# Optimization experiments

Hardware: AMD Instinct MI355X
Metric: run time of the kernel (lower is better)

The kernel has to match this reference:

```python
import jax, jax.numpy as jnp
import numpy as np

IH, IW = 14, 14
NUM_HEADS = 16
HEAD_DIMS = 32
INP_DIMS = 512
B = 128


def make_relative_position_index(ih, iw):
    coords = np.stack(np.meshgrid(np.arange(ih), np.arange(iw), indexing='ij'))  # [2, ih, iw]
    cf = coords.reshape(2, -1)  # [2, n]
    rel = cf[:, :, None] - cf[:, None, :]  # [2, n, n]
    rel = rel.transpose(1, 2, 0)  # [n, n, 2]
    rel[:, :, 0] += ih - 1
    rel[:, :, 1] += iw - 1
    rel[:, :, 0] *= 2 * iw - 1
    return rel.sum(-1).astype(np.int64)  # [n, n]


def setup_inputs() -> dict:
    key = jax.random.key(0)
    k1, k2, k3, k4, k5 = jax.random.split(key, 5)
    n = IH * IW
    inner = NUM_HEADS * HEAD_DIMS
    x = jax.random.normal(k1, (B, n, INP_DIMS), dtype=jnp.float32)
    qkv_w = jax.random.normal(k2, (INP_DIMS, 3 * inner), dtype=jnp.float32) * 0.02
    rel_bias_table = jax.random.normal(k3, ((2 * IH - 1) * (2 * IW - 1), NUM_HEADS), dtype=jnp.float32) * 0.02
    proj_w = jax.random.normal(k4, (inner, INP_DIMS), dtype=jnp.float32) * 0.02
    proj_b = jax.random.normal(k5, (INP_DIMS,), dtype=jnp.float32) * 0.02
    rel_pos_index = jnp.asarray(make_relative_position_index(IH, IW))
    return {"x": x, "qkv_w": qkv_w, "rel_bias_table": rel_bias_table,
            "proj_w": proj_w, "proj_b": proj_b, "rel_pos_index": rel_pos_index}


def reference(x, qkv_w, rel_bias_table, proj_w, proj_b, rel_pos_index):
    b, n, c = x.shape
    h, hd = NUM_HEADS, HEAD_DIMS
    scale = (INP_DIMS // NUM_HEADS) ** (-0.5)
    qkv = x @ qkv_w  # [b, n, 3*h*hd]
    qkv = qkv.reshape(b, n, 3, h, hd).transpose(2, 0, 3, 1, 4)  # [3, b, h, n, hd]
    q, k, v = qkv[0] * scale, qkv[1], qkv[2]
    attn = jnp.einsum('bhqd,bhkd->bhqk', q, k)  # [b, h, n, n]
    # gather relative position bias: [n*n, h] -> [h, n, n]
    bias = rel_bias_table[rel_pos_index.reshape(-1)].reshape(n, n, h).transpose(2, 0, 1)
    attn = jax.nn.softmax(attn + bias[None], axis=-1)
    out = jnp.einsum('bhqk,bhkd->bhqd', attn, v)  # [b, h, n, hd]
    out = out.transpose(0, 2, 1, 3).reshape(b, n, h * hd)
    return out @ proj_w + proj_b
```

## Files before the change

### kernel.cpp

```cpp
#include <hip/hip_runtime.h>

#define NTOK 196
#define QPAD 208
#define KP 208
#define PSTR 232
#define VKP 208

typedef __attribute__((ext_vector_type(8))) short short8;
typedef __attribute__((ext_vector_type(4))) short short4_t;
typedef __attribute__((ext_vector_type(4))) float float4_t;

__device__ __forceinline__ short f2bf(float f) {
  unsigned u = __float_as_uint(f);
  u = (u + 0x7fffu + ((u >> 16) & 1u)) >> 16;
  return (short)u;
}

__global__ __launch_bounds__(256) void fill_kernel(float* __restrict__ out,
                                                   int n) {
  int i = blockIdx.x * 256 + threadIdx.x;
  if (i < n) out[i] = 1000.0f;
}

__global__ __launch_bounds__(256) void cvt_kernel(const float* __restrict__ in,
                                                  short* __restrict__ out) {
  int i = (blockIdx.x * 256 + threadIdx.x) * 8;
  float4_t a = *(const float4_t*)&in[i];
  float4_t b = *(const float4_t*)&in[i + 4];
  short8 v;
  v[0] = f2bf(a[0]); v[1] = f2bf(a[1]); v[2] = f2bf(a[2]); v[3] = f2bf(a[3]);
  v[4] = f2bf(b[0]); v[5] = f2bf(b[1]); v[6] = f2bf(b[2]); v[7] = f2bf(b[3]);
  *(short8*)&out[i] = v;
}

__device__ __forceinline__ void transpose_body(const float* __restrict__ in,
                                               short* __restrict__ out, int R,
                                               int C, int bx, int by,
                                               float (*tile)[65]) {
  int c0 = bx * 64, r0 = by * 64;
  int tc = threadIdx.x & 63, tr = threadIdx.x >> 6;
#pragma unroll
  for (int s = 0; s < 16; s++) {
    int r = s * 4 + tr;
    tile[r][tc] = in[(r0 + r) * C + c0 + tc];
  }
  __syncthreads();
#pragma unroll
  for (int s = 0; s < 16; s++) {
    int i = s * 4 + tr;
    out[(c0 + i) * R + r0 + tc] = f2bf(tile[tc][i]);
  }
}

__global__ __launch_bounds__(256) void prep_kernel(
    const float* __restrict__ qkv_w, const float* __restrict__ proj_w,
    const float* __restrict__ table, const int* __restrict__ rpi,
    short* __restrict__ wt1, short* __restrict__ wt2, float* __restrict__ bias,
    short* __restrict__ vb, int do_vpad) {
  __shared__ float tile[64][65];
  int blk = blockIdx.x;
  if (blk < 192) {
    transpose_body(qkv_w, wt1, 512, 1536, blk % 24, blk / 24, tile);
  } else if (blk < 256) {
    int i = blk - 192;
    transpose_body(proj_w, wt2, 512, 512, i % 8, i / 8, tile);
  } else if (blk < 2960) {
    int idx = (blk - 256) * 256 + threadIdx.x;
    int h = idx / (QPAD * KP);
    int rem = idx % (QPAD * KP);
    int q = rem / KP, k = rem % KP;
    float v = 0.f;
    if (q < NTOK && k < NTOK) v = table[rpi[q * NTOK + k] * 16 + h];
    bias[idx] = v;
  } else if (do_vpad) {
    int i = (blk - 2960) * 256 + threadIdx.x;
    int row = i / 3, g = i - 3 * (i / 3);
    short4_t z = {0, 0, 0, 0};
    *(short4_t*)&vb[row * VKP + 196 + g * 4] = z;
  }
}

__device__ __forceinline__ void gemm_tile(const short* __restrict__ A,
                                          const short* __restrict__ B, int K,
                                          int m0, int n0, short (*As)[72],
                                          short (*Bs)[72], float4_t acc[4][4]) {
  int tid = threadIdx.x;
  int lane = tid & 63, wave = tid >> 6;
  int quad = lane >> 4, l16 = lane & 15;
  int wm = (wave >> 1) * 64, wn = (wave & 1) * 64;
  int srow = tid >> 3, scol = (tid & 7) * 8;
  for (int k0 = 0; k0 < K; k0 += 64) {
#pragma unroll
    for (int i = 0; i < 4; i++) {
      int r = srow + i * 32;
      *(short8*)&As[r][scol] = *(const short8*)&A[(m0 + r) * K + k0 + scol];
      *(short8*)&Bs[r][scol] = *(const short8*)&B[(n0 + r) * K + k0 + scol];
    }
    __syncthreads();
#pragma unroll
    for (int ks = 0; ks < 2; ks++) {
      short8 af[4], bfr[4];
#pragma unroll
      for (int i = 0; i < 4; i++) {
        af[i] = *(short8*)&As[wm + i * 16 + l16][ks * 32 + quad * 8];
        bfr[i] = *(short8*)&Bs[wn + i * 16 + l16][ks * 32 + quad * 8];
      }
#pragma unroll
      for (int mi = 0; mi < 4; mi++)
#pragma unroll
        for (int ni = 0; ni < 4; ni++)
          acc[mi][ni] = __builtin_amdgcn_mfma_f32_16x16x32_bf16(
              af[mi], bfr[ni], acc[mi][ni], 0, 0, 0);
    }
    __syncthreads();
  }
}

__global__ __launch_bounds__(256) void qkv_gemm(
    const short* __restrict__ xb, const short* __restrict__ wt1,
    short* __restrict__ qb, short* __restrict__ kb, short* __restrict__ vb) {
  __shared__ __align__(16) short As[128][72];
  __shared__ __align__(16) short Bs[128][72];
  float4_t acc[4][4];
  float4_t z = {0.f, 0.f, 0.f, 0.f};
#pragma unroll
  for (int i = 0; i < 4; i++)
#pragma unroll
    for (int j = 0; j < 4; j++) acc[i][j] = z;
  int lin = blockIdx.x + blockIdx.y * 12;
  int xcd = lin & 7, loc = lin >> 3;
  int nl = xcd * 294 + loc;
  int bx = nl % 12, by = nl / 12;
  int m0 = by * 128, n0 = bx * 128;
  gemm_tile(xb, wt1, 512, m0, n0, As, Bs, acc);
  int lane = threadIdx.x & 63, wave = threadIdx.x >> 6;
  int quad = lane >> 4, l16 = lane & 15;
  int wm = (wave >> 1) * 64, wn = (wave & 1) * 64;
  const float qscale = 0.17677669529663687f;
#pragma unroll
  for (int mi = 0; mi < 4; mi++)
#pragma unroll
    for (int ni = 0; ni < 4; ni++) {
      int colg = n0 + wn + ni * 16 + l16;
      int s = colg >> 9, rem = colg & 511;
      int h = rem >> 5, d = rem & 31;
      int rowg0 = m0 + wm + mi * 16 + quad * 4;
      if (s == 2) {
        int b = rowg0 / NTOK, nt = rowg0 - b * NTOK;
        short4_t v4;
        v4[0] = f2bf(acc[mi][ni][0]);
        v4[1] = f2bf(acc[mi][ni][1]);
        v4[2] = f2bf(acc[mi][ni][2]);
        v4[3] = f2bf(acc[mi][ni][3]);
        *(short4_t*)&vb[((b * 16 + h) * 32 + d) * VKP + nt] = v4;
      } else {
#pragma unroll
        for (int r = 0; r < 4; r++) {
          int rowg = rowg0 + r;
          int b = rowg / NTOK, n = rowg - b * NTOK;
          int off = ((b * 16 + h) * QPAD + n) * 32 + d;
          if (s == 0)
            qb[off] = f2bf(acc[mi][ni][r] * qscale);
          else
            kb[off] = f2bf(acc[mi][ni][r]);
        }
      }
    }
}

__global__ __launch_bounds__(512) void attn_kernel(
    const short* __restrict__ qb, const short* __restrict__ kb,
    const short* __restrict__ vb, const float* __restrict__ bias,
    short* __restrict__ aout) {
  __shared__ __align__(16) short vT[32][PSTR];
  __shared__ __align__(16) short P[8][16][PSTR];
  int bh = blockIdx.x, b = bh >> 4, h = bh & 15;
  int tid = threadIdx.x, wave = tid >> 6, lane = tid & 63;
  int quad = lane >> 4, l16 = lane & 15;
  int base_row = b * NTOK;
  const short* vsrc = vb + bh * 32 * VKP;
  for (int i = tid; i < 32 * 26; i += 512) {
    int d = i / 26, c = (i - d * 26) * 8;
    *(short8*)&vT[d][c] = *(const short8*)&vsrc[d * VKP + c];
  }
  short8 z8 = {0, 0, 0, 0, 0, 0, 0, 0};
  if (tid < 32 * 3) {
    int d = tid / 3, c = 208 + (tid - d * 3) * 8;
    *(short8*)&vT[d][c] = z8;
  }
  __syncthreads();
  float4_t z4 = {0.f, 0.f, 0.f, 0.f};
  for (int i2 = 0; i2 < 2; i2++) {
    int qt = wave + 8 * i2;
    if (qt > 12) break;
    int qr0 = qt * 16;
    short8 qf = *(const short8*)&qb[(bh * QPAD + qr0 + l16) * 32 + quad * 8];
    float4_t s[13];
#pragma unroll
    for (int kt = 0; kt < 13; kt++) {
      short8 kf =
          *(const short8*)&kb[(bh * QPAD + kt * 16 + l16) * 32 + quad * 8];
      s[kt] = __builtin_amdgcn_mfma_f32_16x16x32_bf16(qf, kf, z4, 0, 0, 0);
    }
    const float* brow = bias + (h * QPAD + qr0 + quad * 4) * KP;
#pragma unroll
    for (int kt = 0; kt < 13; kt++) {
      int col = kt * 16 + l16;
#pragma unroll
      for (int r = 0; r < 4; r++) s[kt][r] += brow[r * KP + col];
    }
    if (l16 >= 4) {
#pragma unroll
      for (int r = 0; r < 4; r++) s[12][r] = -1e30f;
    }
    float invr[4];
#pragma unroll
    for (int r = 0; r < 4; r++) {
      float m = s[0][r];
#pragma unroll
      for (int kt = 1; kt < 13; kt++) m = fmaxf(m, s[kt][r]);
      m = fmaxf(m, __shfl_xor(m, 8, 16));
      m = fmaxf(m, __shfl_xor(m, 4, 16));
      m = fmaxf(m, __shfl_xor(m, 2, 16));
      m = fmaxf(m, __shfl_xor(m, 1, 16));
      float sum = 0.f;
#pragma unroll
      for (int kt = 0; kt < 13; kt++) {
        float p = __expf(s[kt][r] - m);
        s[kt][r] = p;
        sum += p;
      }
      sum += __shfl_xor(sum, 8, 16);
      sum += __shfl_xor(sum, 4, 16);
      sum += __shfl_xor(sum, 2, 16);
      sum += __shfl_xor(sum, 1, 16);
      invr[r] = 1.f / sum;
      short* prow = &P[wave][quad * 4 + r][0];
#pragma unroll
      for (int kt = 0; kt < 13; kt++)
        prow[kt * 16 + l16] = f2bf(s[kt][r]);
      prow[208 + l16] = 0;
    }
    float4_t o0 = z4, o1 = z4;
#pragma unroll
    for (int kt = 0; kt < 7; kt++) {
      short8 pf = *(short8*)&P[wave][l16][kt * 32 + quad * 8];
      short8 vf0 = *(short8*)&vT[l16][kt * 32 + quad * 8];
      short8 vf1 = *(short8*)&vT[16 + l16][kt * 32 + quad * 8];
      o0 = __builtin_amdgcn_mfma_f32_16x16x32_bf16(pf, vf0, o0, 0, 0, 0);
      o1 = __builtin_amdgcn_mfma_f32_16x16x32_bf16(pf, vf1, o1, 0, 0, 0);
    }
#pragma unroll
    for (int r = 0; r < 4; r++) {
      int row = qr0 + quad * 4 + r;
      if (row < NTOK) {
        int off = (base_row + row) * 512 + h * 32;
        aout[off + l16] = f2bf(o0[r] * invr[r]);
        aout[off + 16 + l16] = f2bf(o1[r] * invr[r]);
      }
    }
  }
}

__global__ __launch_bounds__(256, 2) void fused_attn(
    const short* __restrict__ xb, const short* __restrict__ wt1,
    const float* __restrict__ bias, short* __restrict__ aout) {
  __shared__ __align__(16) short R1[64 * PSTR];
  __shared__ __align__(16) short R2[32 * PSTR];
  __shared__ __align__(16) short Qs[224][40];
  __shared__ __align__(16) short Ks[224][40];
  short(*As)[40] = (short(*)[40])R1;
  short(*P)[PSTR] = (short(*)[PSTR])R1;
  short(*Bs)[40] = (short(*)[40])R2;
  short(*vTs)[PSTR] = (short(*)[PSTR])R2;

  int bh = blockIdx.x, b = bh >> 4, h = bh & 15;
  int tid = threadIdx.x, wave = tid >> 6, lane = tid & 63;
  int quad = lane >> 4, l16 = lane & 15;
  int base_row = b * NTOK;

  float4_t z4 = {0.f, 0.f, 0.f, 0.f};
  float4_t acc[4][6];
#pragma unroll
  for (int i = 0; i < 4; i++)
#pragma unroll
    for (int n = 0; n < 6; n++) acc[i][n] = z4;

  int srow = tid >> 2, scol = (tid & 3) * 8;
  for (int k0 = 0; k0 < 512; k0 += 32) {
#pragma unroll
    for (int i = 0; i < 4; i++) {
      int r = srow + i * 64;
      if (r < 224) {
        int gr = base_row + r;
        if (gr > 25087) gr = 25087;
        *(short8*)&As[r][scol] = *(const short8*)&xb[gr * 512 + k0 + scol];
      }
    }
#pragma unroll
    for (int i = 0; i < 2; i++) {
      int r = srow + i * 64;
      if (r < 96) {
        int sec = r >> 5, r32 = r & 31;
        *(short8*)&Bs[r][scol] =
            *(const short8*)&wt1[(sec * 512 + h * 32 + r32) * 512 + k0 + scol];
      }
    }
    __syncthreads();
    short8 af[4], bfv[6];
#pragma unroll
    for (int i = 0; i < 4; i++) {
      int mt = (i < 3) ? (wave + 4 * i) : (12 + (wave & 1));
      af[i] = *(short8*)&As[mt * 16 + l16][quad * 8];
    }
#pragma unroll
    for (int n = 0; n < 6; n++) bfv[n] = *(short8*)&Bs[n * 16 + l16][quad * 8];
#pragma unroll
    for (int i = 0; i < 4; i++)
#pragma unroll
      for (int n = 0; n < 6; n++)
        acc[i][n] = __builtin_amdgcn_mfma_f32_16x16x32_bf16(af[i], bfv[n],
                                                            acc[i][n], 0, 0, 0);
    __syncthreads();
  }
  const float qscale = 0.17677669529663687f;
#pragma unroll
  for (int i = 0; i < 4; i++) {
    if (i == 3 && wave >= 2) break;
    int mt = (i < 3) ? (wave + 4 * i) : (12 + wave);
    int row0 = mt * 16 + quad * 4;
#pragma unroll
    for (int n = 0; n < 6; n++) {
      int c = n * 16 + l16;
#pragma unroll
      for (int r = 0; r < 4; r++) {
        int row = row0 + r;
        float v = acc[i][n][r];
        if (c < 32)
          Qs[row][c] = f2bf(v * qscale);
        else if (c < 64)
          Ks[row][c - 32] = f2bf(v);
        else
          vTs[c - 64][row] = f2bf(v);
      }
    }
  }
  __syncthreads();
  for (int i2 = 0; i2 < 4; i2++) {
    bool active = (i2 < 3) || (wave == 0);
    int qt = (i2 < 3) ? (wave + 4 * i2) : 12;
    int qr0 = qt * 16;
    if (active) {
      short8 qf = *(short8*)&Qs[qr0 + l16][quad * 8];
      float4_t s[13];
#pragma unroll
      for (int kt = 0; kt < 13; kt++) {
        short8 kf = *(short8*)&Ks[kt * 16 + l16][quad * 8];
        s[kt] = __builtin_amdgcn_mfma_f32_16x16x32_bf16(qf, kf, z4, 0, 0, 0);
      }
      const float* brow = bias + (h * QPAD + qr0 + quad * 4) * KP;
#pragma unroll
      for (int kt = 0; kt < 13; kt++) {
        int col = kt * 16 + l16;
#pragma unroll
        for (int r = 0; r < 4; r++) s[kt][r] += brow[r * KP + col];
      }
      if (l16 >= 4) {
#pragma unroll
        for (int r = 0; r < 4; r++) s[12][r] = -1e30f;
      }
      int prow_base = wave * 16 + quad * 4;
#pragma unroll
      for (int r = 0; r < 4; r++) {
        float m = s[0][r];
#pragma unroll
        for (int kt = 1; kt < 13; kt++) m = fmaxf(m, s[kt][r]);
        m = fmaxf(m, __shfl_xor(m, 8, 16));
        m = fmaxf(m, __shfl_xor(m, 4, 16));
        m = fmaxf(m, __shfl_xor(m, 2, 16));
        m = fmaxf(m, __shfl_xor(m, 1, 16));
        float sum = 0.f;
#pragma unroll
        for (int kt = 0; kt < 13; kt++) {
          float p = __expf(s[kt][r] - m);
          s[kt][r] = p;
          sum += p;
        }
        sum += __shfl_xor(sum, 8, 16);
        sum += __shfl_xor(sum, 4, 16);
        sum += __shfl_xor(sum, 2, 16);
        sum += __shfl_xor(sum, 1, 16);
        float inv = 1.f / sum;
        short* prow = &P[prow_base + r][0];
#pragma unroll
        for (int kt = 0; kt < 13; kt++)
          prow[kt * 16 + l16] = f2bf(s[kt][r] * inv);
        prow[208 + l16] = 0;
      }
    }
    __syncthreads();
    if (active) {
      float4_t o0 = z4, o1 = z4;
#pragma unroll
      for (int kt = 0; kt < 7; kt++) {
        short8 pf = *(short8*)&P[wave * 16 + l16][kt * 32 + quad * 8];
        short8 vf0 = *(short8*)&vTs[l16][kt * 32 + quad * 8];
        short8 vf1 = *(short8*)&vTs[16 + l16][kt * 32 + quad * 8];
        o0 = __builtin_amdgcn_mfma_f32_16x16x32_bf16(pf, vf0, o0, 0, 0, 0);
        o1 = __builtin_amdgcn_mfma_f32_16x16x32_bf16(pf, vf1, o1, 0, 0, 0);
      }
#pragma unroll
      for (int r = 0; r < 4; r++) {
        int row = qr0 + quad * 4 + r;
        if (row < NTOK) {
          int off = (base_row + row) * 512 + h * 32;
          aout[off + l16] = f2bf(o0[r]);
          aout[off + 16 + l16] = f2bf(o1[r]);
        }
      }
    }
    __syncthreads();
  }
}

__global__ __launch_bounds__(256) void proj_gemm(
    const short* __restrict__ a, const short* __restrict__ wt,
    const float* __restrict__ pb, float* __restrict__ out) {
  __shared__ __align__(16) short As[128][72];
  __shared__ __align__(16) short Bs[128][72];
  float4_t acc[4][4];
  float4_t z = {0.f, 0.f, 0.f, 0.f};
#pragma unroll
  for (int i = 0; i < 4; i++)
#pragma unroll
    for (int j = 0; j < 4; j++) acc[i][j] = z;
  int lin = blockIdx.x + blockIdx.y * 4;
  int xcd = lin & 7, loc = lin >> 3;
  int nl = xcd * 98 + loc;
  int bx = nl % 4, by = nl / 4;
  int m0 = by * 128, n0 = bx * 128;
  gemm_tile(a, wt, 512, m0, n0, As, Bs, acc);
  int lane = threadIdx.x & 63, wave = threadIdx.x >> 6;
  int quad = lane >> 4, l16 = lane & 15;
  int wm = (wave >> 1) * 64, wn = (wave & 1) * 64;
#pragma unroll
  for (int mi = 0; mi < 4; mi++)
#pragma unroll
    for (int ni = 0; ni < 4; ni++) {
      int colg = n0 + wn + ni * 16 + l16;
      float bv = pb[colg];
#pragma unroll
      for (int r = 0; r < 4; r++) {
        int rowg = m0 + wm + mi * 16 + quad * 4 + r;
        out[rowg * 512 + colg] = acc[mi][ni][r] + bv;
      }
    }
}

extern "C" void kernel_launch(void* const* d_in, const int* in_sizes, int n_in,
                              void* d_out, int out_size, void* d_ws,
                              size_t ws_size, hipStream_t stream) {
  const float* x = (const float*)d_in[0];
  const float* qkv_w = (const float*)d_in[1];
  const float* table = (const float*)d_in[2];
  const float* proj_w = (const float*)d_in[3];
  const float* proj_b = (const float*)d_in[4];
  const int* rpi = (const int*)d_in[5];
  float* out = (float*)d_out;

  char* w = (char*)d_ws;
  short* wt1 = (short*)(w);
  short* wt2 = (short*)(w + 1572864);
  float* bias = (float*)(w + 2097152);
  short* xb = (short*)(w + 4866048);
  short* qb = (short*)(w + 30556160);
  short* kb = (short*)(w + 57819136);
  short* vb = (short*)(w + 85082112);
  const size_t NEEDED_SPLIT = 112345088;
  const size_t NEEDED_FUSED = 30556160 + 25690112;

  int split = ws_size >= NEEDED_SPLIT;
  prep_kernel<<<3728, 256, 0, stream>>>(qkv_w, proj_w, table, rpi, wt1, wt2,
                                        bias, vb, split);
  if (split) {
    short* aout = xb;
    cvt_kernel<<<25088 * 512 / (256 * 8), 256, 0, stream>>>(x, xb);
    qkv_gemm<<<dim3(12, 196), 256, 0, stream>>>(xb, wt1, qb, kb, vb);
    attn_kernel<<<2048, 512, 0, stream>>>(qb, kb, vb, bias, aout);
    proj_gemm<<<dim3(4, 196), 256, 0, stream>>>(aout, wt2, proj_b, out);
  } else if (ws_size >= NEEDED_FUSED) {
    short* aout = (short*)(w + 30556160);
    cvt_kernel<<<25088 * 512 / (256 * 8), 256, 0, stream>>>(x, xb);
    fused_attn<<<2048, 256, 0, stream>>>(xb, wt1, bias, aout);
    proj_gemm<<<dim3(4, 196), 256, 0, stream>>>(aout, wt2, proj_b, out);
  } else {
    fill_kernel<<<(out_size + 255) / 256, 256, 0, stream>>>(out, out_size);
  }
}
```

Measured before the change: 276.0 us.

## Use direct global-to-LDS loads in GEMMs, fold x conversion into prep, shrink attention blocks

The GEMM tile loader now uses global_load_lds to move data straight from global memory into unpadded 64-wide LDS tiles, skipping the trip through registers. The separate fp32-to-bf16 conversion of x becomes extra blocks of the prep kernel, which removes one launch. The attention kernel moves from 512 to 256 threads per block, so each wave handles more query tiles and less LDS is used per block. Dropping the LDS row padding can cause bank conflicts on the fragment reads, and the smaller attention blocks leave fewer waves in flight per block.

```diff
diff --git a/kernel.cpp b/kernel.cpp
--- a/kernel.cpp
+++ b/kernel.cpp
@@ -20,17 +20,6 @@
                                                    int n) {
   int i = blockIdx.x * 256 + threadIdx.x;
   if (i < n) out[i] = 1000.0f;
-}
-
-__global__ __launch_bounds__(256) void cvt_kernel(const float* __restrict__ in,
-                                                  short* __restrict__ out) {
-  int i = (blockIdx.x * 256 + threadIdx.x) * 8;
-  float4_t a = *(const float4_t*)&in[i];
-  float4_t b = *(const float4_t*)&in[i + 4];
-  short8 v;
-  v[0] = f2bf(a[0]); v[1] = f2bf(a[1]); v[2] = f2bf(a[2]); v[3] = f2bf(a[3]);
-  v[4] = f2bf(b[0]); v[5] = f2bf(b[1]); v[6] = f2bf(b[2]); v[7] = f2bf(b[3]);
-  *(short8*)&out[i] = v;
 }
 
 __device__ __forceinline__ void transpose_body(const float* __restrict__ in,
@@ -55,8 +44,9 @@
 __global__ __launch_bounds__(256) void prep_kernel(
     const float* __restrict__ qkv_w, const float* __restrict__ proj_w,
     const float* __restrict__ table, const int* __restrict__ rpi,
-    short* __restrict__ wt1, short* __restrict__ wt2, float* __restrict__ bias,
-    short* __restrict__ vb, int do_vpad) {
+    const float* __restrict__ x, short* __restrict__ wt1,
+    short* __restrict__ wt2, float* __restrict__ bias, short* __restrict__ vb,
+    short* __restrict__ xb, int do_vpad) {
   __shared__ float tile[64][65];
   int blk = blockIdx.x;
   if (blk < 192) {
@@ -72,29 +62,47 @@
     float v = 0.f;
     if (q < NTOK && k < NTOK) v = table[rpi[q * NTOK + k] * 16 + h];
     bias[idx] = v;
-  } else if (do_vpad) {
-    int i = (blk - 2960) * 256 + threadIdx.x;
-    int row = i / 3, g = i - 3 * (i / 3);
-    short4_t z = {0, 0, 0, 0};
-    *(short4_t*)&vb[row * VKP + 196 + g * 4] = z;
+  } else if (blk < 3728) {
+    if (do_vpad) {
+      int i = (blk - 2960) * 256 + threadIdx.x;
+      int row = i / 3, g = i - 3 * (i / 3);
+      short4_t z = {0, 0, 0, 0};
+      *(short4_t*)&vb[row * VKP + 196 + g * 4] = z;
+    }
+  } else {
+    int i = ((blk - 3728) * 256 + threadIdx.x) * 8;
+    float4_t a = *(const float4_t*)&x[i];
+    float4_t b = *(const float4_t*)&x[i + 4];
+    short8 v;
+    v[0] = f2bf(a[0]); v[1] = f2bf(a[1]); v[2] = f2bf(a[2]); v[3] = f2bf(a[3]);
+    v[4] = f2bf(b[0]); v[5] = f2bf(b[1]); v[6] = f2bf(b[2]); v[7] = f2bf(b[3]);
+    *(short8*)&xb[i] = v;
   }
 }
 
 __device__ __forceinline__ void gemm_tile(const short* __restrict__ A,
                                           const short* __restrict__ B, int K,
-                                          int m0, int n0, short (*As)[72],
-                                          short (*Bs)[72], float4_t acc[4][4]) {
+                                          int m0, int n0, short* As, short* Bs,
+                                          float4_t acc[4][4]) {
   int tid = threadIdx.x;
   int lane = tid & 63, wave = tid >> 6;
   int quad = lane >> 4, l16 = lane & 15;
   int wm = (wave >> 1) * 64, wn = (wave & 1) * 64;
-  int srow = tid >> 3, scol = (tid & 7) * 8;
+  int lrow = lane >> 3, lcol = (lane & 7) * 8;
+  const short* Abase = A + m0 * K;
+  const short* Bbase = B + n0 * K;
   for (int k0 = 0; k0 < K; k0 += 64) {
 #pragma unroll
     for (int i = 0; i < 4; i++) {
-      int r = srow + i * 32;
-      *(short8*)&As[r][scol] = *(const short8*)&A[(m0 + r) * K + k0 + scol];
-      *(short8*)&Bs[r][scol] = *(const short8*)&B[(n0 + r) * K + k0 + scol];
+      int r = (wave * 4 + i) * 8;
+      __builtin_amdgcn_global_load_lds(
+          (const __attribute__((address_space(1))) void*)
+              &Abase[(r + lrow) * K + k0 + lcol],
+          (__attribute__((address_space(3))) void*)&As[r * 64], 16, 0, 0);
+      __builtin_amdgcn_global_load_lds(
+          (const __attribute__((address_space(1))) void*)
+              &Bbase[(r + lrow) * K + k0 + lcol],
+          (__attribute__((address_space(3))) void*)&Bs[r * 64], 16, 0, 0);
     }
     __syncthreads();
 #pragma unroll
@@ -102,8 +110,8 @@
       short8 af[4], bfr[4];
 #pragma unroll
       for (int i = 0; i < 4; i++) {
-        af[i] = *(short8*)&As[wm + i * 16 + l16][ks * 32 + quad * 8];
-        bfr[i] = *(short8*)&Bs[wn + i * 16 + l16][ks * 32 + quad * 8];
+        af[i] = *(short8*)&As[(wm + i * 16 + l16) * 64 + ks * 32 + quad * 8];
+        bfr[i] = *(short8*)&Bs[(wn + i * 16 + l16) * 64 + ks * 32 + quad * 8];
       }
 #pragma unroll
       for (int mi = 0; mi < 4; mi++)
@@ -119,8 +127,8 @@
 __global__ __launch_bounds__(256) void qkv_gemm(
     const short* __restrict__ xb, const short* __restrict__ wt1,
     short* __restrict__ qb, short* __restrict__ kb, short* __restrict__ vb) {
-  __shared__ __align__(16) short As[128][72];
-  __shared__ __align__(16) short Bs[128][72];
+  __shared__ __align__(16) short As[128 * 64];
+  __shared__ __align__(16) short Bs[128 * 64];
   float4_t acc[4][4];
   float4_t z = {0.f, 0.f, 0.f, 0.f};
 #pragma unroll
@@ -168,31 +176,32 @@
     }
 }
 
-__global__ __launch_bounds__(512) void attn_kernel(
+__global__ __launch_bounds__(256) void attn_kernel(
     const short* __restrict__ qb, const short* __restrict__ kb,
     const short* __restrict__ vb, const float* __restrict__ bias,
     short* __restrict__ aout) {
   __shared__ __align__(16) short vT[32][PSTR];
-  __shared__ __align__(16) short P[8][16][PSTR];
+  __shared__ __align__(16) short P[4][16][PSTR];
   int bh = blockIdx.x, b = bh >> 4, h = bh & 15;
   int tid = threadIdx.x, wave = tid >> 6, lane = tid & 63;
   int quad = lane >> 4, l16 = lane & 15;
   int base_row = b * NTOK;
   const short* vsrc = vb + bh * 32 * VKP;
-  for (int i = tid; i < 32 * 26; i += 512) {
+  for (int i = tid; i < 32 * 26; i += 256) {
     int d = i / 26, c = (i - d * 26) * 8;
     *(short8*)&vT[d][c] = *(const short8*)&vsrc[d * VKP + c];
   }
   short8 z8 = {0, 0, 0, 0, 0, 0, 0, 0};
-  if (tid < 32 * 3) {
+  if (tid < 96) {
     int d = tid / 3, c = 208 + (tid - d * 3) * 8;
     *(short8*)&vT[d][c] = z8;
   }
   __syncthreads();
   float4_t z4 = {0.f, 0.f, 0.f, 0.f};
-  for (int i2 = 0; i2 < 2; i2++) {
-    int qt = wave + 8 * i2;
-    if (qt > 12) break;
+  for (int i2 = 0; i2 < 4; i2++) {
+    bool active = (i2 < 3) || (wave == 0);
+    if (!active) break;
+    int qt = (i2 < 3) ? (wave + 4 * i2) : 12;
     int qr0 = qt * 16;
     short8 qf = *(const short8*)&qb[(bh * QPAD + qr0 + l16) * 32 + quad * 8];
     float4_t s[13];
@@ -426,8 +435,8 @@
 __global__ __launch_bounds__(256) void proj_gemm(
     const short* __restrict__ a, const short* __restrict__ wt,
     const float* __restrict__ pb, float* __restrict__ out) {
-  __shared__ __align__(16) short As[128][72];
-  __shared__ __align__(16) short Bs[128][72];
+  __shared__ __align__(16) short As[128 * 64];
+  __shared__ __align__(16) short Bs[128 * 64];
   float4_t acc[4][4];
   float4_t z = {0.f, 0.f, 0.f, 0.f};
 #pragma unroll
@@ -480,17 +489,17 @@
   const size_t NEEDED_FUSED = 30556160 + 25690112;
 
   int split = ws_size >= NEEDED_SPLIT;
-  prep_kernel<<<3728, 256, 0, stream>>>(qkv_w, proj_w, table, rpi, wt1, wt2,
-                                        bias, vb, split);
+  if (ws_size >= NEEDED_FUSED) {
+    prep_kernel<<<10000, 256, 0, stream>>>(qkv_w, proj_w, table, rpi, x, wt1,
+                                           wt2, bias, vb, xb, split);
+  }
   if (split) {
     short* aout = xb;
-    cvt_kernel<<<25088 * 512 / (256 * 8), 256, 0, stream>>>(x, xb);
     qkv_gemm<<<dim3(12, 196), 256, 0, stream>>>(xb, wt1, qb, kb, vb);
-    attn_kernel<<<2048, 512, 0, stream>>>(qb, kb, vb, bias, aout);
+    attn_kernel<<<2048, 256, 0, stream>>>(qb, kb, vb, bias, aout);
     proj_gemm<<<dim3(4, 196), 256, 0, stream>>>(aout, wt2, proj_b, out);
   } else if (ws_size >= NEEDED_FUSED) {
     short* aout = (short*)(w + 30556160);
-    cvt_kernel<<<25088 * 512 / (256 * 8), 256, 0, stream>>>(x, xb);
     fused_attn<<<2048, 256, 0, stream>>>(xb, wt1, bias, aout);
     proj_gemm<<<dim3(4, 196), 256, 0, stream>>>(aout, wt2, proj_b, out);
   } else {
```

Result: no change. 274.9 us (-0.4%).
